# Kernel tuning notes

Measured on AMD Instinct MI355X. Metric: run time of the kernel, lower is better.

The kernel has to match this reference:

```python
import jax, jax.numpy as jnp
import numpy as np
import math

LOG_2PI = math.log(2.0 * math.pi)


def setup_inputs() -> dict:
    key = jax.random.key(0)
    k_x, k_mu = jax.random.split(key, 2)
    B, T, S, M, D = 8, 4096, 64, 8, 128
    return {
        "X": jax.random.normal(k_x, (B, T, D), dtype=jnp.float32),
        "pi_logits": jnp.zeros((S,), dtype=jnp.float32),
        "trans_logits": jnp.zeros((S, S), dtype=jnp.float32),
        "weight_logits": jnp.zeros((S, M), dtype=jnp.float32),
        "means": jax.random.normal(k_mu, (S, M, D), dtype=jnp.float32),
        "log_vars": jnp.zeros((S, M, D), dtype=jnp.float32),
    }


def reference(X, pi_logits, trans_logits, weight_logits, means, log_vars):
    # X: [B,T,D]; means/log_vars: [S,M,D]
    D = X.shape[-1]
    inv_vars = jnp.exp(-log_vars)                                   # [S,M,D]
    # -0.5 * sum_d (x_d - mu_d)^2 / var_d, expanded as GEMMs (same math):
    a = jnp.einsum('btd,smd->btsm', X * X, inv_vars)                # sum x^2/var
    b = jnp.einsum('btd,smd->btsm', X, means * inv_vars)            # sum x*mu/var
    c = jnp.sum(means * means * inv_vars, axis=-1)                  # [S,M]
    exp_term = -0.5 * (a - 2.0 * b + c[None, None, :, :])           # [B,T,S,M]
    log_norm = -0.5 * (jnp.sum(log_vars, axis=-1) + D * LOG_2PI)    # [S,M]
    log_mix_w = jax.nn.log_softmax(weight_logits, axis=1)           # [S,M]
    # emission log-prob per state: logsumexp over mixture components
    emis = jax.scipy.special.logsumexp(
        exp_term + (log_norm + log_mix_w)[None, None], axis=-1)     # [B,T,S]

    log_pi = jax.nn.log_softmax(pi_logits)                          # [S]
    log_A = jax.nn.log_softmax(trans_logits, axis=1)                # [S,S]

    alpha0 = log_pi[None, :] + emis[:, 0]                           # [B,S]
    emis_t = jnp.swapaxes(emis, 0, 1)                               # [T,B,S]

    def step(alpha, e_t):
        # alpha: [B,S]; log-semiring matvec: logsumexp_i(alpha_i + A_ij)
        nxt = e_t + jax.scipy.special.logsumexp(
            alpha[:, :, None] + log_A[None, :, :], axis=1)
        return nxt, None

    alpha_T, _ = jax.lax.scan(step, alpha0, emis_t[1:])
    return jax.scipy.special.logsumexp(alpha_T, axis=-1)            # [B]
```

## Files before the change

kernel.cpp:

```cpp
#include <hip/hip_runtime.h>
#include <hip/hip_bf16.h>
#include <math.h>

#define LOG2PI_F 1.8378770664093453f

typedef __attribute__((ext_vector_type(8))) short bf16x8;
typedef __attribute__((ext_vector_type(4))) float f32x4;
typedef __attribute__((ext_vector_type(16))) float f32x16;

static __device__ inline short f2bf(float x) {
  __hip_bfloat16 h = __float2bfloat16(x);
  return *reinterpret_cast<short*>(&h);
}
static __device__ inline unsigned cvtpk(float lo, float hi) {
  unsigned r;
  asm("v_cvt_pk_bf16_f32 %0, %1, %2" : "=v"(r) : "v"(lo), "v"(hi));
  return r;
}
static __device__ inline f32x4 mfma16(bf16x8 a, bf16x8 b, f32x4 c) {
  return __builtin_amdgcn_mfma_f32_16x16x32_bf16(a, b, c, 0, 0, 0);
}
static __device__ inline f32x16 mfma32(bf16x8 a, bf16x8 b, f32x16 c) {
  return __builtin_amdgcn_mfma_f32_32x32x16_bf16(a, b, c, 0, 0, 0);
}

__global__ __launch_bounds__(256) void mmm_prep_fused(
    const float* __restrict__ tl, const float* __restrict__ means,
    const float* __restrict__ log_vars, const float* __restrict__ weight_logits,
    const float* __restrict__ X,
    short* __restrict__ WTbf, short* __restrict__ Gt,
    float* __restrict__ const_c, short* __restrict__ XeP) {
  __shared__ float red[4];
  int bid = blockIdx.x;
  int tid = threadIdx.x;

  if (bid < 64) {
    if (tid < 64) {
      int r = bid, lane = tid;
      float v = tl[r * 64 + lane];
      float mx = v;
      #pragma unroll
      for (int off = 1; off < 64; off <<= 1) mx = fmaxf(mx, __shfl_xor(mx, off));
      float e = expf(v - mx);
      float s = e;
      #pragma unroll
      for (int off = 1; off < 64; off <<= 1) s += __shfl_xor(s, off);
      WTbf[lane * 64 + r] = f2bf(e / s);
    }
    return;
  }

  if (bid < 320) {
    int h = tid >> 7, d = tid & 127;
    int sm = (bid - 64) * 2 + h;
    int s = sm >> 3, m = sm & 7;
    float lv = log_vars[sm * 128 + d];
    float iv = expf(-lv);
    float mu = means[sm * 128 + d];
    float miv = mu * iv;
    Gt[sm * 256 + d] = f2bf(miv);
    Gt[sm * 256 + 128 + d] = f2bf(-0.5f * iv);
    float v = mu * miv + lv;
    #pragma unroll
    for (int off = 1; off < 64; off <<= 1) v += __shfl_xor(v, off);
    if ((tid & 63) == 0) red[tid >> 6] = v;
    __syncthreads();
    if (d == 0) {
      float tot = red[2 * h] + red[2 * h + 1];
      float wl[8];
      float mx = -3.4e38f;
      #pragma unroll
      for (int j = 0; j < 8; ++j) { wl[j] = weight_logits[s * 8 + j]; mx = fmaxf(mx, wl[j]); }
      float sum = 0.f;
      #pragma unroll
      for (int j = 0; j < 8; ++j) sum += expf(wl[j] - mx);
      float lmw = wl[m] - mx - logf(sum);
      const_c[sm] = -0.5f * (tot + 128.0f * LOG2PI_F) + lmw;
    }
    return;
  }

  int kbid = bid - 320;
  int q = kbid >> 7;
  int bt = ((kbid & 127) << 8) + tid;
  const float4* src = (const float4*)(X + (size_t)bt * 128 + q * 32);
  float xv[32];
  #pragma unroll
  for (int i = 0; i < 8; ++i) {
    float4 v = src[i];
    xv[4 * i] = v.x; xv[4 * i + 1] = v.y; xv[4 * i + 2] = v.z; xv[4 * i + 3] = v.w;
  }
  size_t base1 = ((size_t)q * 32768 + bt) * 32;
  size_t base2 = ((size_t)(q + 4) * 32768 + bt) * 32;
  int bx = bt & 3;
  #pragma unroll
  for (int g = 0; g < 4; ++g) {
    unsigned w1[4], w2[4];
    #pragma unroll
    for (int j = 0; j < 4; ++j) {
      float a = xv[g * 8 + 2 * j], c = xv[g * 8 + 2 * j + 1];
      w1[j] = cvtpk(a, c);
      w2[j] = cvtpk(a * a, c * c);
    }
    int gs = (g ^ bx) * 8;
    *(uint4*)&XeP[base1 + gs] = *(uint4*)w1;
    *(uint4*)&XeP[base2 + gs] = *(uint4*)w2;
  }
}

__global__ __launch_bounds__(512) void mmm_emis_kernel(
    const short* __restrict__ Gt, const short* __restrict__ XeP,
    const float* __restrict__ const_c,
    float* __restrict__ ehat, float* __restrict__ cmax) {
  __shared__ __align__(16) short Bt[16384];
  __shared__ __align__(16) float ccs[512];
  __shared__ float wavemax[8][64];
  __shared__ float colmax[64];
  int tid = threadIdx.x;
  int w = tid >> 6, lane = tid & 63, lr = lane & 15, lg = lane >> 4;

  ccs[tid] = const_c[tid];

  bf16x8 gf[4][8];
  #pragma unroll
  for (int rt = 0; rt < 4; ++rt) {
    int row = w * 64 + rt * 16 + lr;
    #pragma unroll
    for (int kc = 0; kc < 8; ++kc)
      gf[rt][kc] = *(const bf16x8*)&Gt[row * 256 + kc * 32 + lg * 8];
  }

  uint4 sreg[4];
  {
    size_t bt0 = (size_t)blockIdx.x * 64;
    #pragma unroll
    for (int r = 0; r < 4; ++r) {
      int ofs = r * 8192 + tid * 16;
      int kb2 = ofs >> 12, rem = ofs & 4095;
      sreg[r] = *(const uint4*)((const char*)XeP + ((size_t)kb2 * 32768 + bt0) * 64 + rem);
    }
  }

  for (int it = 0; it < 2; ++it) {
    int bt0 = (blockIdx.x + it * 256) * 64;
    __syncthreads();
    #pragma unroll
    for (int r = 0; r < 4; ++r)
      *(uint4*)((char*)Bt + r * 8192 + tid * 16) = sreg[r];
    __syncthreads();
    if (it == 0) {
      size_t bt0n = ((size_t)blockIdx.x + 256) * 64;
      #pragma unroll
      for (int r = 0; r < 4; ++r) {
        int ofs = r * 8192 + tid * 16;
        int kb2 = ofs >> 12, rem = ofs & 4095;
        sreg[r] = *(const uint4*)((const char*)XeP + ((size_t)kb2 * 32768 + bt0n) * 64 + rem);
      }
    }

    f32x4 acc[4][4];
    #pragma unroll
    for (int rt = 0; rt < 4; ++rt)
      #pragma unroll
      for (int ct = 0; ct < 4; ++ct)
        acc[rt][ct] = (f32x4){0.f, 0.f, 0.f, 0.f};

    #pragma unroll
    for (int kc = 0; kc < 8; ++kc) {
      bf16x8 bfr[4];
      #pragma unroll
      for (int ct = 0; ct < 4; ++ct) {
        int btL = ct * 16 + lr;
        bfr[ct] = *(const bf16x8*)&Bt[kc * 2048 + btL * 32 + ((lg ^ (btL & 3)) * 8)];
      }
      #pragma unroll
      for (int rt = 0; rt < 4; ++rt)
        #pragma unroll
        for (int ct = 0; ct < 4; ++ct)
          acc[rt][ct] = mfma16(gf[rt][kc], bfr[ct], acc[rt][ct]);
    }

    float lse[4][4];
    #pragma unroll
    for (int rt = 0; rt < 4; ++rt) {
      f32x4 cc = *(f32x4*)&ccs[w * 64 + rt * 16 + lg * 4];
      #pragma unroll
      for (int ct = 0; ct < 4; ++ct) {
        f32x4 v = acc[rt][ct] + cc;
        float mx = fmaxf(fmaxf(v[0], v[1]), fmaxf(v[2], v[3]));
        mx = fmaxf(mx, __shfl_xor(mx, 16));
        float sum = expf(v[0] - mx) + expf(v[1] - mx) + expf(v[2] - mx) + expf(v[3] - mx);
        sum += __shfl_xor(sum, 16);
        lse[rt][ct] = mx + logf(sum);
      }
    }
    #pragma unroll
    for (int ct = 0; ct < 4; ++ct) {
      float cm = fmaxf(fmaxf(lse[0][ct], lse[1][ct]), fmaxf(lse[2][ct], lse[3][ct]));
      cm = fmaxf(cm, __shfl_xor(cm, 32));
      if (lg == 0) wavemax[w][ct * 16 + lr] = cm;
    }
    __syncthreads();
    if (w == 0) {
      float cm = wavemax[0][lane];
      #pragma unroll
      for (int ww = 1; ww < 8; ++ww) cm = fmaxf(cm, wavemax[ww][lane]);
      colmax[lane] = cm;
      cmax[(size_t)bt0 + lane] = cm;
    }
    __syncthreads();
    #pragma unroll
    for (int ct = 0; ct < 4; ++ct) {
      float cm = colmax[ct * 16 + lr];
      #pragma unroll
      for (int rt = 0; rt < 4; ++rt) {
        float v = expf(lse[rt][ct] - cm);
        if (!(lg & 1))
          ehat[((size_t)bt0 + ct * 16 + lr) * 64 + (w * 8 + rt * 2 + (lg >> 1))] = v;
      }
    }
  }
}

__global__ __launch_bounds__(64) void mmm_chunk_kernel(
    const short* __restrict__ WTbf, const float* __restrict__ ehat,
    const float* __restrict__ cmax, float* __restrict__ NT,
    float* __restrict__ aux) {
  __shared__ __align__(16) float elds[1024];
  int chunk = blockIdx.x, b = blockIdx.y;
  int lane = threadIdx.x;
  int l31 = lane & 31, hi = lane >> 5;

  int t0 = (chunk == 0) ? 1 : chunk * 16;
  int nsteps = (chunk == 0) ? 15 : 16;
  const float* eb = ehat + (size_t)b * 4096 * 64;

  {
    const float* esrc = eb + (size_t)t0 * 64;
    #pragma unroll
    for (int r = 0; r < 4; ++r)
      *(f32x4*)&elds[r * 256 + lane * 4] = *(const f32x4*)&esrc[r * 256 + lane * 4];
  }

  bf16x8 af[2][4];
  #pragma unroll
  for (int wi = 0; wi < 2; ++wi)
    #pragma unroll
    for (int kb = 0; kb < 4; ++kb)
      af[wi][kb] = *(const bf16x8*)&WTbf[(wi * 32 + l31) * 64 + kb * 16 + hi * 8];

  unsigned P[2][2][4][2];
  #pragma unroll
  for (int s = 0; s < 2; ++s) {
    int col = s * 32 + l31;
    #pragma unroll
    for (int cm = 0; cm < 2; ++cm)
      #pragma unroll
      for (int q = 0; q < 4; ++q)
        #pragma unroll
        for (int p = 0; p < 2; ++p) {
          int row = 32 * cm + 8 * q + 4 * hi + 2 * p;
          unsigned lo = (row == col) ? 0x3F80u : 0u;
          unsigned h16 = (row + 1 == col) ? 0x3F80u : 0u;
          P[s][cm][q][p] = lo | (h16 << 16);
        }
  }

  __syncthreads();

  float logscale = 0.f;
  f32x4 ecur[2][4], enxt[2][4];
  #pragma unroll
  for (int cm = 0; cm < 2; ++cm)
    #pragma unroll
    for (int q = 0; q < 4; ++q)
      ecur[cm][q] = *(const f32x4*)&elds[cm * 32 + q * 8 + hi * 4];

  for (int it = 0; it < nsteps; ++it) {
    if (it + 1 < nsteps) {
      #pragma unroll
      for (int cm = 0; cm < 2; ++cm)
        #pragma unroll
        for (int q = 0; q < 4; ++q)
          enxt[cm][q] = *(const f32x4*)&elds[(it + 1) * 64 + cm * 32 + q * 8 + hi * 4];
    }

    __builtin_amdgcn_s_setprio(1);
    #pragma unroll
    for (int s = 0; s < 2; ++s) {
      bf16x8 B[4];
      #pragma unroll
      for (int kb = 0; kb < 4; ++kb) {
        int cm = kb >> 1, kbl = kb & 1;
        int4 wrd;
        #pragma unroll
        for (int p = 0; p < 2; ++p) {
          unsigned avv = P[s][cm][2 * kbl + 1][p];
          unsigned bvv = P[s][cm][2 * kbl][p];
          asm("v_permlane32_swap_b32 %0, %1" : "+v"(avv), "+v"(bvv));
          if (p == 0) { wrd.x = (int)bvv; wrd.z = (int)avv; }
          else        { wrd.y = (int)bvv; wrd.w = (int)avv; }
        }
        B[kb] = *(bf16x8*)&wrd;
      }

      f32x16 d0, d1;
      #pragma unroll
      for (int r = 0; r < 16; ++r) { d0[r] = 0.f; d1[r] = 0.f; }
      #pragma unroll
      for (int kb = 0; kb < 4; ++kb) {
        d0 = mfma32(af[0][kb], B[kb], d0);
        d1 = mfma32(af[1][kb], B[kb], d1);
      }

      #pragma unroll
      for (int q = 0; q < 4; ++q)
        #pragma unroll
        for (int p = 0; p < 2; ++p) {
          P[s][0][q][p] = cvtpk(d0[4 * q + 2 * p] * ecur[0][q][2 * p],
                                d0[4 * q + 2 * p + 1] * ecur[0][q][2 * p + 1]);
          P[s][1][q][p] = cvtpk(d1[4 * q + 2 * p] * ecur[1][q][2 * p],
                                d1[4 * q + 2 * p + 1] * ecur[1][q][2 * p + 1]);
        }
    }
    __builtin_amdgcn_s_setprio(0);

    if ((it & 7) == 7) {
      float m = 0.f;
      #pragma unroll
      for (int s = 0; s < 2; ++s)
        #pragma unroll
        for (int cm = 0; cm < 2; ++cm)
          #pragma unroll
          for (int q = 0; q < 4; ++q)
            #pragma unroll
            for (int p = 0; p < 2; ++p) {
              unsigned u = P[s][cm][q][p];
              m = fmaxf(m, __uint_as_float(u << 16));
              m = fmaxf(m, __uint_as_float(u & 0xffff0000u));
            }
      #pragma unroll
      for (int off = 1; off < 64; off <<= 1) m = fmaxf(m, __shfl_xor(m, off));
      float inv = 1.0f / m;
      #pragma unroll
      for (int s = 0; s < 2; ++s)
        #pragma unroll
        for (int cm = 0; cm < 2; ++cm)
          #pragma unroll
          for (int q = 0; q < 4; ++q)
            #pragma unroll
            for (int p = 0; p < 2; ++p) {
              unsigned u = P[s][cm][q][p];
              P[s][cm][q][p] = cvtpk(__uint_as_float(u << 16) * inv,
                                     __uint_as_float(u & 0xffff0000u) * inv);
            }
      logscale += logf(m);
    }

    #pragma unroll
    for (int cm = 0; cm < 2; ++cm)
      #pragma unroll
      for (int q = 0; q < 4; ++q) ecur[cm][q] = enxt[cm][q];
  }

  float* No = NT + (((size_t)b * 256 + chunk) << 12);
  #pragma unroll
  for (int s = 0; s < 2; ++s)
    #pragma unroll
    for (int cm = 0; cm < 2; ++cm)
      #pragma unroll
      for (int q = 0; q < 4; ++q)
        #pragma unroll
        for (int p = 0; p < 2; ++p) {
          int row = 32 * cm + 8 * q + 4 * hi + 2 * p;
          int col = s * 32 + l31;
          unsigned u = P[s][cm][q][p];
          No[row * 64 + col] = __uint_as_float(u << 16);
          No[(row + 1) * 64 + col] = __uint_as_float(u & 0xffff0000u);
        }

  float cs = (lane < nsteps) ? cmax[(size_t)b * 4096 + t0 + lane] : 0.f;
  #pragma unroll
  for (int off = 1; off < 64; off <<= 1) cs += __shfl_xor(cs, off);
  if (lane == 0) aux[(size_t)b * 256 + chunk] = cs + logscale;
}

__global__ __launch_bounds__(256) void mmm_merge_kernel(
    const float* __restrict__ NT, const float* __restrict__ aux,
    float* __restrict__ G2T, float* __restrict__ auxg) {
  int g = blockIdx.x, b = blockIdx.y;
  int tid = threadIdx.x;
  int w = tid >> 6, lane = tid & 63;
  int wi = w >> 1, wj = w & 1;
  int lr = lane & 15, lg = lane >> 4;

  __shared__ __align__(16) short L[2][4096];
  __shared__ float wmax[4];

  for (int idx = tid; idx < 4096; idx += 256) {
    int j = idx >> 6, k = idx & 63;
    L[0][idx ^ ((j & 7) << 3)] = (j == k) ? (short)0x3F80 : (short)0;
  }
  __syncthreads();

  int cbase = b * 256 + g * 16;

  float logscale = 0.f;
  int cur = 0;
  f32x4 acc[2][2];

  f32x4 apre[2][2][2];
  {
    const float* Mc = NT + ((size_t)cbase << 12);
    #pragma unroll
    for (int rt = 0; rt < 2; ++rt)
      #pragma unroll
      for (int kc = 0; kc < 2; ++kc) {
        const float* src = Mc + (wi * 32 + rt * 16 + lr) * 64 + kc * 32 + lg * 8;
        apre[rt][kc][0] = *(const f32x4*)src;
        apre[rt][kc][1] = *(const f32x4*)(src + 4);
      }
  }

  for (int cc = 0; cc < 16; ++cc) {
    f32x4 acur[2][2][2];
    #pragma unroll
    for (int rt = 0; rt < 2; ++rt)
      #pragma unroll
      for (int kc = 0; kc < 2; ++kc) {
        acur[rt][kc][0] = apre[rt][kc][0];
        acur[rt][kc][1] = apre[rt][kc][1];
      }
    if (cc < 15) {
      const float* Mc = NT + ((size_t)(cbase + cc + 1) << 12);
      #pragma unroll
      for (int rt = 0; rt < 2; ++rt)
        #pragma unroll
        for (int kc = 0; kc < 2; ++kc) {
          const float* src = Mc + (wi * 32 + rt * 16 + lr) * 64 + kc * 32 + lg * 8;
          apre[rt][kc][0] = *(const f32x4*)src;
          apre[rt][kc][1] = *(const f32x4*)(src + 4);
        }
    }

    logscale += aux[cbase + cc];

    bf16x8 afr[2][2];
    #pragma unroll
    for (int rt = 0; rt < 2; ++rt)
      #pragma unroll
      for (int kc = 0; kc < 2; ++kc) {
        unsigned fw[4];
        fw[0] = cvtpk(acur[rt][kc][0][0], acur[rt][kc][0][1]);
        fw[1] = cvtpk(acur[rt][kc][0][2], acur[rt][kc][0][3]);
        fw[2] = cvtpk(acur[rt][kc][1][0], acur[rt][kc][1][1]);
        fw[3] = cvtpk(acur[rt][kc][1][2], acur[rt][kc][1][3]);
        afr[rt][kc] = *(bf16x8*)fw;
      }

    bf16x8 bfr[2][2];
    #pragma unroll
    for (int ct = 0; ct < 2; ++ct) {
      int j = wj * 32 + ct * 16 + lr;
      int sw = (j & 7) << 3;
      #pragma unroll
      for (int kc = 0; kc < 2; ++kc)
        bfr[ct][kc] = *(const bf16x8*)&L[cur][(j * 64 + kc * 32 + lg * 8) ^ sw];
    }

    #pragma unroll
    for (int rt = 0; rt < 2; ++rt)
      #pragma unroll
      for (int ct = 0; ct < 2; ++ct) {
        f32x4 c = {0.f, 0.f, 0.f, 0.f};
        c = mfma16(afr[rt][0], bfr[ct][0], c);
        c = mfma16(afr[rt][1], bfr[ct][1], c);
        acc[rt][ct] = c;
      }

    float m = 0.f;
    #pragma unroll
    for (int rt = 0; rt < 2; ++rt)
      #pragma unroll
      for (int ct = 0; ct < 2; ++ct)
        #pragma unroll
        for (int r = 0; r < 4; ++r) m = fmaxf(m, acc[rt][ct][r]);
    #pragma unroll
    for (int off = 1; off < 64; off <<= 1) m = fmaxf(m, __shfl_xor(m, off));
    if (lane == 0) wmax[w] = m;
    __syncthreads();
    m = fmaxf(fmaxf(wmax[0], wmax[1]), fmaxf(wmax[2], wmax[3]));
    float inv = 1.0f / m;
    #pragma unroll
    for (int rt = 0; rt < 2; ++rt)
      #pragma unroll
      for (int ct = 0; ct < 2; ++ct) acc[rt][ct] *= inv;
    logscale += logf(m);

    int nxt = cur ^ 1;
    unsigned* L32 = (unsigned*)&L[nxt][0];
    #pragma unroll
    for (int rt = 0; rt < 2; ++rt)
      #pragma unroll
      for (int ct = 0; ct < 2; ++ct) {
        int row0 = wi * 32 + rt * 16 + lg * 4;
        int col = wj * 32 + ct * 16 + lr;
        int sidx = (col * 64 + row0) ^ ((col & 7) << 3);
        L32[(sidx >> 1) + 0] = cvtpk(acc[rt][ct][0], acc[rt][ct][1]);
        L32[(sidx >> 1) + 1] = cvtpk(acc[rt][ct][2], acc[rt][ct][3]);
      }
    __syncthreads();
    cur = nxt;
  }

  float* Mo = G2T + (((size_t)b * 16 + g) << 12);
  #pragma unroll
  for (int rt = 0; rt < 2; ++rt)
    #pragma unroll
    for (int ct = 0; ct < 2; ++ct)
      #pragma unroll
      for (int r = 0; r < 4; ++r) {
        int row = wi * 32 + rt * 16 + lg * 4 + r;
        int col = wj * 32 + ct * 16 + lr;
        Mo[row * 64 + col] = acc[rt][ct][r];
      }

  if (w == 0 && lane == 0) auxg[b * 16 + g] = logscale;
}

__global__ __launch_bounds__(64) void mmm_combine_kernel(
    const float* __restrict__ pi_logits, const float* __restrict__ ehat,
    const float* __restrict__ cmax, const float* __restrict__ G2T,
    const float* __restrict__ auxg, float* __restrict__ out) {
  int b = blockIdx.x, lane = threadIdx.x;
  __shared__ __align__(16) float alds[64];

  float pv = pi_logits[lane];
  float mx = pv;
  #pragma unroll
  for (int off = 1; off < 64; off <<= 1) mx = fmaxf(mx, __shfl_xor(mx, off));
  float pe = expf(pv - mx);
  float ps = pe;
  #pragma unroll
  for (int off = 1; off < 64; off <<= 1) ps += __shfl_xor(ps, off);

  float a = (pe / ps) * ehat[(size_t)b * 4096 * 64 + lane];
  double logtot = (double)cmax[(size_t)b * 4096];
  alds[lane] = a;
  __builtin_amdgcn_wave_barrier();

  const float* Mb = G2T + (((size_t)b * 16) << 12) + lane * 64;
  f32x4 mc[16], mn[16];
  #pragma unroll
  for (int i = 0; i < 16; ++i) mc[i] = *(const f32x4*)&Mb[i * 4];

  for (int g = 0; g < 16; ++g) {
    if (g < 15) {
      const float* Mn = Mb + ((size_t)(g + 1) << 12);
      #pragma unroll
      for (int i = 0; i < 16; ++i) mn[i] = *(const f32x4*)&Mn[i * 4];
    }
    f32x4 a4 = {0.f, 0.f, 0.f, 0.f};
    #pragma unroll
    for (int i = 0; i < 16; ++i) {
      f32x4 av = *(const f32x4*)&alds[i * 4];
      a4 += mc[i] * av;
    }
    float acc = (a4[0] + a4[1]) + (a4[2] + a4[3]);
    float s = acc;
    #pragma unroll
    for (int off = 1; off < 64; off <<= 1) s += __shfl_xor(s, off);
    logtot += (double)(auxg[b * 16 + g] + logf(s));
    float an = acc / s;
    __builtin_amdgcn_wave_barrier();
    alds[lane] = an;
    __builtin_amdgcn_wave_barrier();
    #pragma unroll
    for (int i = 0; i < 16; ++i) mc[i] = mn[i];
  }
  if (lane == 0) out[b] = (float)logtot;
}

extern "C" void kernel_launch(void* const* d_in, const int* in_sizes, int n_in,
                              void* d_out, int out_size, void* d_ws, size_t ws_size,
                              hipStream_t stream) {
  const float* X      = (const float*)d_in[0];
  const float* pi_l   = (const float*)d_in[1];
  const float* tr_l   = (const float*)d_in[2];
  const float* wl     = (const float*)d_in[3];
  const float* means  = (const float*)d_in[4];
  const float* lvs    = (const float*)d_in[5];
  float* out = (float*)d_out;

  float* ws = (float*)d_ws;
  short* Gt      = (short*)ws;
  float* const_c = ws + 65536;
  short* WTbf    = (short*)(ws + 66048);
  float* cmaxp   = ws + 68608;
  float* ehat    = ws + 101376;
  short* XeP     = (short*)(ws + 2198528);
  float* NT      = ws + 2198528;
  float* aux     = ws + 10587136;
  float* G2T     = ws + 10591232;
  float* auxg    = ws + 11115520;

  mmm_prep_fused<<<832, 256, 0, stream>>>(tr_l, means, lvs, wl, X,
                                          WTbf, Gt, const_c, XeP);
  mmm_emis_kernel<<<256, 512, 0, stream>>>(Gt, XeP, const_c, ehat, cmaxp);
  mmm_chunk_kernel<<<dim3(256, 8), 64, 0, stream>>>(WTbf, ehat, cmaxp, NT, aux);
  mmm_merge_kernel<<<dim3(16, 8), 256, 0, stream>>>(NT, aux, G2T, auxg);
  mmm_combine_kernel<<<8, 64, 0, stream>>>(pi_l, ehat, cmaxp, G2T, auxg, out);
}
```

Measured before the change: 112.8 us.

## Halve chunk length, store chunk products in bf16, rescale merge less often

The chunk kernel now covers 8 time steps per chunk instead of 16, which doubles the grid to 512×8 blocks and shortens each block's serial MFMA chain. It writes its 64×64 chunk matrices as bf16 instead of fp32. The merge kernel then loads bf16 fragments directly and skips the conversion, and it normalises by the max only every 4 products, with 32 groups per batch. The combine kernel walks 32 group matrices instead of 16, so its serial chain is longer, and rescaling less often raises the risk of bf16 overflow or underflow.

```diff
diff --git a/kernel.cpp b/kernel.cpp
--- a/kernel.cpp
+++ b/kernel.cpp
@@ -222,23 +222,23 @@
   }
 }
 
-__global__ __launch_bounds__(64) void mmm_chunk_kernel(
+__global__ __launch_bounds__(64, 4) void mmm_chunk_kernel(
     const short* __restrict__ WTbf, const float* __restrict__ ehat,
-    const float* __restrict__ cmax, float* __restrict__ NT,
+    const float* __restrict__ cmax, short* __restrict__ NTb,
     float* __restrict__ aux) {
-  __shared__ __align__(16) float elds[1024];
+  __shared__ __align__(16) float elds[512];
   int chunk = blockIdx.x, b = blockIdx.y;
   int lane = threadIdx.x;
   int l31 = lane & 31, hi = lane >> 5;
 
-  int t0 = (chunk == 0) ? 1 : chunk * 16;
-  int nsteps = (chunk == 0) ? 15 : 16;
+  int t0 = (chunk == 0) ? 1 : chunk * 8;
+  int nsteps = (chunk == 0) ? 7 : 8;
   const float* eb = ehat + (size_t)b * 4096 * 64;
 
   {
     const float* esrc = eb + (size_t)t0 * 64;
     #pragma unroll
-    for (int r = 0; r < 4; ++r)
+    for (int r = 0; r < 2; ++r)
       *(f32x4*)&elds[r * 256 + lane * 4] = *(const f32x4*)&esrc[r * 256 + lane * 4];
   }
 
@@ -269,21 +269,14 @@
   __syncthreads();
 
   float logscale = 0.f;
-  f32x4 ecur[2][4], enxt[2][4];
-  #pragma unroll
-  for (int cm = 0; cm < 2; ++cm)
-    #pragma unroll
-    for (int q = 0; q < 4; ++q)
-      ecur[cm][q] = *(const f32x4*)&elds[cm * 32 + q * 8 + hi * 4];
 
   for (int it = 0; it < nsteps; ++it) {
-    if (it + 1 < nsteps) {
-      #pragma unroll
-      for (int cm = 0; cm < 2; ++cm)
-        #pragma unroll
-        for (int q = 0; q < 4; ++q)
-          enxt[cm][q] = *(const f32x4*)&elds[(it + 1) * 64 + cm * 32 + q * 8 + hi * 4];
-    }
+    f32x4 ev[2][4];
+    #pragma unroll
+    for (int cm = 0; cm < 2; ++cm)
+      #pragma unroll
+      for (int q = 0; q < 4; ++q)
+        ev[cm][q] = *(const f32x4*)&elds[it * 64 + cm * 32 + q * 8 + hi * 4];
 
     __builtin_amdgcn_s_setprio(1);
     #pragma unroll
@@ -317,10 +310,10 @@
       for (int q = 0; q < 4; ++q)
         #pragma unroll
         for (int p = 0; p < 2; ++p) {
-          P[s][0][q][p] = cvtpk(d0[4 * q + 2 * p] * ecur[0][q][2 * p],
-                                d0[4 * q + 2 * p + 1] * ecur[0][q][2 * p + 1]);
-          P[s][1][q][p] = cvtpk(d1[4 * q + 2 * p] * ecur[1][q][2 * p],
-                                d1[4 * q + 2 * p + 1] * ecur[1][q][2 * p + 1]);
+          P[s][0][q][p] = cvtpk(d0[4 * q + 2 * p] * ev[0][q][2 * p],
+                                d0[4 * q + 2 * p + 1] * ev[0][q][2 * p + 1]);
+          P[s][1][q][p] = cvtpk(d1[4 * q + 2 * p] * ev[1][q][2 * p],
+                                d1[4 * q + 2 * p + 1] * ev[1][q][2 * p + 1]);
         }
     }
     __builtin_amdgcn_s_setprio(0);
@@ -356,14 +349,9 @@
             }
       logscale += logf(m);
     }
-
-    #pragma unroll
-    for (int cm = 0; cm < 2; ++cm)
-      #pragma unroll
-      for (int q = 0; q < 4; ++q) ecur[cm][q] = enxt[cm][q];
-  }
-
-  float* No = NT + (((size_t)b * 256 + chunk) << 12);
+  }
+
+  unsigned short* No = (unsigned short*)(NTb + (((size_t)b * 512 + chunk) << 12));
   #pragma unroll
   for (int s = 0; s < 2; ++s)
     #pragma unroll
@@ -375,18 +363,18 @@
           int row = 32 * cm + 8 * q + 4 * hi + 2 * p;
           int col = s * 32 + l31;
           unsigned u = P[s][cm][q][p];
-          No[row * 64 + col] = __uint_as_float(u << 16);
-          No[(row + 1) * 64 + col] = __uint_as_float(u & 0xffff0000u);
+          No[row * 64 + col] = (unsigned short)(u & 0xffffu);
+          No[(row + 1) * 64 + col] = (unsigned short)(u >> 16);
         }
 
   float cs = (lane < nsteps) ? cmax[(size_t)b * 4096 + t0 + lane] : 0.f;
   #pragma unroll
   for (int off = 1; off < 64; off <<= 1) cs += __shfl_xor(cs, off);
-  if (lane == 0) aux[(size_t)b * 256 + chunk] = cs + logscale;
+  if (lane == 0) aux[(size_t)b * 512 + chunk] = cs + logscale;
 }
 
 __global__ __launch_bounds__(256) void mmm_merge_kernel(
-    const float* __restrict__ NT, const float* __restrict__ aux,
+    const short* __restrict__ NTb, const float* __restrict__ aux,
     float* __restrict__ G2T, float* __restrict__ auxg) {
   int g = blockIdx.x, b = blockIdx.y;
   int tid = threadIdx.x;
@@ -403,60 +391,38 @@
   }
   __syncthreads();
 
-  int cbase = b * 256 + g * 16;
+  int cbase = b * 512 + g * 16;
 
   float logscale = 0.f;
   int cur = 0;
   f32x4 acc[2][2];
 
-  f32x4 apre[2][2][2];
+  bf16x8 apre[2][2];
   {
-    const float* Mc = NT + ((size_t)cbase << 12);
+    const short* Mc = NTb + ((size_t)cbase << 12);
     #pragma unroll
     for (int rt = 0; rt < 2; ++rt)
       #pragma unroll
-      for (int kc = 0; kc < 2; ++kc) {
-        const float* src = Mc + (wi * 32 + rt * 16 + lr) * 64 + kc * 32 + lg * 8;
-        apre[rt][kc][0] = *(const f32x4*)src;
-        apre[rt][kc][1] = *(const f32x4*)(src + 4);
-      }
+      for (int kc = 0; kc < 2; ++kc)
+        apre[rt][kc] = *(const bf16x8*)&Mc[(wi * 32 + rt * 16 + lr) * 64 + kc * 32 + lg * 8];
   }
 
   for (int cc = 0; cc < 16; ++cc) {
-    f32x4 acur[2][2][2];
+    bf16x8 acur[2][2];
     #pragma unroll
     for (int rt = 0; rt < 2; ++rt)
       #pragma unroll
-      for (int kc = 0; kc < 2; ++kc) {
-        acur[rt][kc][0] = apre[rt][kc][0];
-        acur[rt][kc][1] = apre[rt][kc][1];
-      }
+      for (int kc = 0; kc < 2; ++kc) acur[rt][kc] = apre[rt][kc];
     if (cc < 15) {
-      const float* Mc = NT + ((size_t)(cbase + cc + 1) << 12);
+      const short* Mc = NTb + ((size_t)(cbase + cc + 1) << 12);
       #pragma unroll
       for (int rt = 0; rt < 2; ++rt)
         #pragma unroll
-        for (int kc = 0; kc < 2; ++kc) {
-          const float* src = Mc + (wi * 32 + rt * 16 + lr) * 64 + kc * 32 + lg * 8;
-          apre[rt][kc][0] = *(const f32x4*)src;
-          apre[rt][kc][1] = *(const f32x4*)(src + 4);
-        }
+        for (int kc = 0; kc < 2; ++kc)
+          apre[rt][kc] = *(const bf16x8*)&Mc[(wi * 32 + rt * 16 + lr) * 64 + kc * 32 + lg * 8];
     }
 
     logscale += aux[cbase + cc];
-
-    bf16x8 afr[2][2];
-    #pragma unroll
-    for (int rt = 0; rt < 2; ++rt)
-      #pragma unroll
-      for (int kc = 0; kc < 2; ++kc) {
-        unsigned fw[4];
-        fw[0] = cvtpk(acur[rt][kc][0][0], acur[rt][kc][0][1]);
-        fw[1] = cvtpk(acur[rt][kc][0][2], acur[rt][kc][0][3]);
-        fw[2] = cvtpk(acur[rt][kc][1][0], acur[rt][kc][1][1]);
-        fw[3] = cvtpk(acur[rt][kc][1][2], acur[rt][kc][1][3]);
-        afr[rt][kc] = *(bf16x8*)fw;
-      }
 
     bf16x8 bfr[2][2];
     #pragma unroll
@@ -473,29 +439,31 @@
       #pragma unroll
       for (int ct = 0; ct < 2; ++ct) {
         f32x4 c = {0.f, 0.f, 0.f, 0.f};
-        c = mfma16(afr[rt][0], bfr[ct][0], c);
-        c = mfma16(afr[rt][1], bfr[ct][1], c);
+        c = mfma16(acur[rt][0], bfr[ct][0], c);
+        c = mfma16(acur[rt][1], bfr[ct][1], c);
         acc[rt][ct] = c;
       }
 
-    float m = 0.f;
-    #pragma unroll
-    for (int rt = 0; rt < 2; ++rt)
-      #pragma unroll
-      for (int ct = 0; ct < 2; ++ct)
-        #pragma unroll
-        for (int r = 0; r < 4; ++r) m = fmaxf(m, acc[rt][ct][r]);
-    #pragma unroll
-    for (int off = 1; off < 64; off <<= 1) m = fmaxf(m, __shfl_xor(m, off));
-    if (lane == 0) wmax[w] = m;
-    __syncthreads();
-    m = fmaxf(fmaxf(wmax[0], wmax[1]), fmaxf(wmax[2], wmax[3]));
-    float inv = 1.0f / m;
-    #pragma unroll
-    for (int rt = 0; rt < 2; ++rt)
-      #pragma unroll
-      for (int ct = 0; ct < 2; ++ct) acc[rt][ct] *= inv;
-    logscale += logf(m);
+    if ((cc & 3) == 3) {
+      float m = 0.f;
+      #pragma unroll
+      for (int rt = 0; rt < 2; ++rt)
+        #pragma unroll
+        for (int ct = 0; ct < 2; ++ct)
+          #pragma unroll
+          for (int r = 0; r < 4; ++r) m = fmaxf(m, acc[rt][ct][r]);
+      #pragma unroll
+      for (int off = 1; off < 64; off <<= 1) m = fmaxf(m, __shfl_xor(m, off));
+      if (lane == 0) wmax[w] = m;
+      __syncthreads();
+      m = fmaxf(fmaxf(wmax[0], wmax[1]), fmaxf(wmax[2], wmax[3]));
+      float inv = 1.0f / m;
+      #pragma unroll
+      for (int rt = 0; rt < 2; ++rt)
+        #pragma unroll
+        for (int ct = 0; ct < 2; ++ct) acc[rt][ct] *= inv;
+      logscale += logf(m);
+    }
 
     int nxt = cur ^ 1;
     unsigned* L32 = (unsigned*)&L[nxt][0];
@@ -513,7 +481,7 @@
     cur = nxt;
   }
 
-  float* Mo = G2T + (((size_t)b * 16 + g) << 12);
+  float* Mo = G2T + (((size_t)b * 32 + g) << 12);
   #pragma unroll
   for (int rt = 0; rt < 2; ++rt)
     #pragma unroll
@@ -525,7 +493,7 @@
         Mo[row * 64 + col] = acc[rt][ct][r];
       }
 
-  if (w == 0 && lane == 0) auxg[b * 16 + g] = logscale;
+  if (w == 0 && lane == 0) auxg[b * 32 + g] = logscale;
 }
 
 __global__ __launch_bounds__(64) void mmm_combine_kernel(
@@ -549,13 +517,13 @@
   alds[lane] = a;
   __builtin_amdgcn_wave_barrier();
 
-  const float* Mb = G2T + (((size_t)b * 16) << 12) + lane * 64;
+  const float* Mb = G2T + (((size_t)b * 32) << 12) + lane * 64;
   f32x4 mc[16], mn[16];
   #pragma unroll
   for (int i = 0; i < 16; ++i) mc[i] = *(const f32x4*)&Mb[i * 4];
 
-  for (int g = 0; g < 16; ++g) {
-    if (g < 15) {
+  for (int g = 0; g < 32; ++g) {
+    if (g < 31) {
       const float* Mn = Mb + ((size_t)(g + 1) << 12);
       #pragma unroll
       for (int i = 0; i < 16; ++i) mn[i] = *(const f32x4*)&Mn[i * 4];
@@ -570,7 +538,7 @@
     float s = acc;
     #pragma unroll
     for (int off = 1; off < 64; off <<= 1) s += __shfl_xor(s, off);
-    logtot += (double)(auxg[b * 16 + g] + logf(s));
+    logtot += (double)(auxg[b * 32 + g] + logf(s));
     float an = acc / s;
     __builtin_amdgcn_wave_barrier();
     alds[lane] = an;
@@ -599,15 +567,15 @@
   float* cmaxp   = ws + 68608;
   float* ehat    = ws + 101376;
   short* XeP     = (short*)(ws + 2198528);
-  float* NT      = ws + 2198528;
+  short* NTb     = (short*)(ws + 2198528);
   float* aux     = ws + 10587136;
   float* G2T     = ws + 10591232;
-  float* auxg    = ws + 11115520;
+  float* auxg    = ws + 11639808;
 
   mmm_prep_fused<<<832, 256, 0, stream>>>(tr_l, means, lvs, wl, X,
                                           WTbf, Gt, const_c, XeP);
   mmm_emis_kernel<<<256, 512, 0, stream>>>(Gt, XeP, const_c, ehat, cmaxp);
-  mmm_chunk_kernel<<<dim3(256, 8), 64, 0, stream>>>(WTbf, ehat, cmaxp, NT, aux);
-  mmm_merge_kernel<<<dim3(16, 8), 256, 0, stream>>>(NT, aux, G2T, auxg);
+  mmm_chunk_kernel<<<dim3(512, 8), 64, 0, stream>>>(WTbf, ehat, cmaxp, NTb, aux);
+  mmm_merge_kernel<<<dim3(32, 8), 256, 0, stream>>>(NTb, aux, G2T, auxg);
   mmm_combine_kernel<<<8, 64, 0, stream>>>(pi_l, ehat, cmaxp, G2T, auxg, out);
 }
```

Measured after the change: 130.9 us. 16.0% more time.
